# Kernel optimization log

Measured on AMD Instinct MI355X. Metric: run time of the kernel, lower is better.

Reference implementation:

```python
import jax, jax.numpy as jnp
import numpy as np

N_CUST = 500000
N_FUND = 50000
N_EDGE = 4000000
D_CUST = 101
D_FUND = 1
HID = 64


def setup_inputs() -> dict:
    key = jax.random.key(0)
    ks = jax.random.split(key, 16)
    s = lambda fan_in: 1.0 / np.sqrt(fan_in)
    return {
        "x_customer": jax.random.normal(ks[0], (N_CUST, D_CUST), jnp.float32),
        "x_fund": jax.random.normal(ks[1], (N_FUND, D_FUND), jnp.float32),
        "src_fund": jax.random.randint(ks[2], (N_EDGE,), 0, N_FUND, jnp.int64),
        "dst_customer": jax.random.randint(ks[3], (N_EDGE,), 0, N_CUST, jnp.int64),
        # per-node-type input projections
        "W_cust": jax.random.uniform(ks[4], (D_CUST, HID), jnp.float32, -s(D_CUST), s(D_CUST)),
        "b_cust": jax.random.uniform(ks[5], (HID,), jnp.float32, -s(D_CUST), s(D_CUST)),
        "W_fund": jax.random.uniform(ks[6], (D_FUND, HID), jnp.float32, -s(D_FUND), s(D_FUND)),
        "b_fund": jax.random.uniform(ks[7], (HID,), jnp.float32, -s(D_FUND), s(D_FUND)),
        # SAGEConv fund->customer: lin_l (neighbor aggr, bias) + lin_r (self, no bias)
        "W_l": jax.random.uniform(ks[8], (HID, HID), jnp.float32, -s(HID), s(HID)),
        "b_l": jax.random.uniform(ks[9], (HID,), jnp.float32, -s(HID), s(HID)),
        "W_r": jax.random.uniform(ks[10], (HID, HID), jnp.float32, -s(HID), s(HID)),
        # output head
        "W_out": jax.random.uniform(ks[11], (HID, 2), jnp.float32, -s(HID), s(HID)),
        "b_out": jax.random.uniform(ks[12], (2,), jnp.float32, -s(HID), s(HID)),
    }


def reference(x_customer, x_fund, src_fund, dst_customer,
              W_cust, b_cust, W_fund, b_fund, W_l, b_l, W_r, W_out, b_out):
    # per-node-type linear + relu
    h_c = jax.nn.relu(x_customer @ W_cust + b_cust)  # [N_CUST, HID]
    h_f = jax.nn.relu(x_fund @ W_fund + b_fund)      # [N_FUND, HID]

    # SAGEConv (fund -> customer): gather src fund features per edge,
    # mean-aggregate by destination customer (scatter-sum / count)
    msgs = h_f[src_fund]  # [N_EDGE, HID]
    summed = jax.ops.segment_sum(msgs, dst_customer, num_segments=N_CUST)
    cnt = jax.ops.segment_sum(jnp.ones((msgs.shape[0],), msgs.dtype),
                              dst_customer, num_segments=N_CUST)
    mean = summed / jnp.maximum(cnt, 1.0)[:, None]

    out_c = mean @ W_l + b_l + h_c @ W_r  # SAGE: lin_l(aggr) + lin_r(self)
    return out_c @ W_out + b_out          # [N_CUST, 2]
```

## Files before the change

kernel.cpp:

```cpp
#include <hip/hip_runtime.h>
#include <stdint.h>

#define N_CUST 500000
#define N_FUND 50000
#define N_EDGE 4000000
#define D_CUST 101
#define HID 64

#define NB   512
#define EPB  ((N_EDGE + NB - 1) / NB)
#define CB   1024
#define NBKT ((N_CUST + CB - 1) / CB)
#define TILES (N_CUST / 16)

typedef float  float4u __attribute__((ext_vector_type(4), aligned(4)));
using frag_ab = __attribute__((ext_vector_type(8))) short;
using frag_cd = __attribute__((ext_vector_type(4))) float;

struct __align__(16) Accum { float g0, g1, cnt, pad; };

__device__ __forceinline__ short f2bf(float f) {
    unsigned u = __float_as_uint(f);
    u += 0x7fffu + ((u >> 16) & 1u);
    return (short)(u >> 16);
}

__global__ __launch_bounds__(256) void k_prep(
    const float* __restrict__ W_r, const float* __restrict__ W_out,
    const float* __restrict__ b_l, const float* __restrict__ b_out,
    const float* __restrict__ W_l,
    float* __restrict__ Bt, float* __restrict__ Af, float* __restrict__ c2)
{
    int t = threadIdx.x;
    if (t < 128) {
        int h = t >> 1, j = t & 1;
        float s = 0.f, sa = 0.f;
        for (int k = 0; k < 64; ++k) {
            float wo = W_out[k * 2 + j];
            s  = fmaf(W_r[h * 64 + k], wo, s);
            sa = fmaf(W_l[h * 64 + k], wo, sa);
        }
        Bt[t] = s;
        Af[t] = sa;
    } else if (t < 130) {
        int j = t - 128;
        float s = b_out[j];
        for (int k = 0; k < 64; ++k)
            s = fmaf(b_l[k], W_out[k * 2 + j], s);
        c2[j] = s;
    }
}

__global__ __launch_bounds__(256) void k_gf(
    const float* __restrict__ x_fund,
    const float* __restrict__ W_fund,
    const float* __restrict__ b_fund,
    const float* __restrict__ Af,
    float2* __restrict__ gf)
{
    int f = blockIdx.x * 256 + threadIdx.x;
    if (f >= N_FUND) return;
    float xf = x_fund[f];
    float g0 = 0.f, g1 = 0.f;
    #pragma unroll
    for (int h = 0; h < 64; ++h) {
        float hf = fmaxf(fmaf(xf, W_fund[h], b_fund[h]), 0.f);
        g0 = fmaf(hf, Af[2 * h + 0], g0);
        g1 = fmaf(hf, Af[2 * h + 1], g1);
    }
    gf[f] = make_float2(g0, g1);
}

__global__ __launch_bounds__(256) void k_count(
    const int* __restrict__ dst, unsigned* __restrict__ cntTab)
{
    __shared__ unsigned hist[NBKT];
    int t = threadIdx.x, b = blockIdx.x;
    for (int k = t; k < NBKT; k += 256) hist[k] = 0;
    __syncthreads();
    int e0 = b * EPB, e1 = min(e0 + EPB, N_EDGE);
    for (int e = e0 + t; e < e1; e += 256)
        atomicAdd(&hist[((unsigned)dst[e]) >> 10], 1u);
    __syncthreads();
    for (int k = t; k < NBKT; k += 256) cntTab[(size_t)k * NB + b] = hist[k];
}

__global__ __launch_bounds__(256) void k_scan1(
    const unsigned* __restrict__ cntTab, unsigned* __restrict__ bktBase)
{
    __shared__ unsigned tot[NBKT];
    int t = threadIdx.x;
    for (int k = t; k < NBKT; k += 256) {
        unsigned s = 0;
        const unsigned* row = cntTab + (size_t)k * NB;
        for (int b = 0; b < NB; ++b) s += row[b];
        tot[k] = s;
    }
    __syncthreads();
    if (t < 64) {
        unsigned v[8], pre[8], run = 0;
        #pragma unroll
        for (int j = 0; j < 8; ++j) {
            int idx = t * 8 + j;
            v[j] = (idx < NBKT) ? tot[idx] : 0u;
            pre[j] = run; run += v[j];
        }
        unsigned sc = run;
        #pragma unroll
        for (int d = 1; d < 64; d <<= 1) {
            unsigned n = __shfl_up(sc, d, 64);
            if (t >= d) sc += n;
        }
        unsigned lane_excl = sc - run;
        #pragma unroll
        for (int j = 0; j < 8; ++j) {
            int idx = t * 8 + j;
            if (idx < NBKT) bktBase[idx] = lane_excl + pre[j];
        }
        if (t == 0) bktBase[NBKT] = N_EDGE;
    }
}

__global__ __launch_bounds__(64) void k_scan2(
    const unsigned* __restrict__ cntTab, const unsigned* __restrict__ bktBase,
    unsigned* __restrict__ offTab)
{
    int k = blockIdx.x, l = threadIdx.x;
    const unsigned* row = cntTab + (size_t)k * NB;
    unsigned v[8], pre[8], run = 0;
    #pragma unroll
    for (int j = 0; j < 8; ++j) { v[j] = row[l * 8 + j]; pre[j] = run; run += v[j]; }
    unsigned sc = run;
    #pragma unroll
    for (int d = 1; d < 64; d <<= 1) {
        unsigned n = __shfl_up(sc, d, 64);
        if (l >= d) sc += n;
    }
    unsigned base = bktBase[k] + (sc - run);
    unsigned* orow = offTab + (size_t)k * NB;
    #pragma unroll
    for (int j = 0; j < 8; ++j) orow[l * 8 + j] = base + pre[j];
}

__global__ __launch_bounds__(256) void k_reorder(
    const int* __restrict__ src, const int* __restrict__ dst,
    const unsigned* __restrict__ offTab, unsigned* __restrict__ recs)
{
    __shared__ unsigned cur[NBKT];
    int t = threadIdx.x, b = blockIdx.x;
    for (int k = t; k < NBKT; k += 256) cur[k] = offTab[(size_t)k * NB + b];
    __syncthreads();
    int e0 = b * EPB, e1 = min(e0 + EPB, N_EDGE);
    for (int e = e0 + t; e < e1; e += 256) {
        unsigned d = (unsigned)dst[e];
        unsigned s = (unsigned)src[e];
        unsigned pos = atomicAdd(&cur[d >> 10], 1u);
        recs[pos] = s | ((d & 1023u) << 16);
    }
}

__global__ __launch_bounds__(256) void k_aggregate(
    const unsigned* __restrict__ recs, const unsigned* __restrict__ bktBase,
    const float2* __restrict__ gf, float2* __restrict__ mean)
{
    __shared__ float s0[CB], s1[CB], scn[CB];
    int t = threadIdx.x, k = blockIdx.x;
    for (int c = t; c < CB; c += 256) { s0[c] = 0.f; s1[c] = 0.f; scn[c] = 0.f; }
    __syncthreads();
    unsigned r0 = bktBase[k], r1 = bktBase[k + 1];
    for (unsigned i = r0 + t; i < r1; i += 256) {
        unsigned r = recs[i];
        float2 g = gf[r & 0xFFFFu];
        unsigned dl = r >> 16;
        atomicAdd(&s0[dl], g.x);
        atomicAdd(&s1[dl], g.y);
        atomicAdd(&scn[dl], 1.f);
    }
    __syncthreads();
    int cust0 = k * CB;
    for (int c = t; c < CB; c += 256) {
        int cu = cust0 + c;
        if (cu < N_CUST) {
            float inv = 1.0f / fmaxf(scn[c], 1.0f);
            mean[cu] = make_float2(s0[c] * inv, s1[c] * inv);
        }
    }
}

__global__ __launch_bounds__(256) void k_scatter_direct(
    const int* __restrict__ src, const int* __restrict__ dst,
    const float2* __restrict__ gf, Accum* __restrict__ A)
{
    int stride = gridDim.x * 256;
    for (int e = blockIdx.x * 256 + threadIdx.x; e < N_EDGE; e += stride) {
        int s = src[e], d = dst[e];
        float2 g = gf[s];
        unsafeAtomicAdd(&A[d].g0, g.x);
        unsafeAtomicAdd(&A[d].g1, g.y);
        unsafeAtomicAdd(&A[d].cnt, 1.0f);
    }
}

template<bool USE_MEAN>
__global__ __launch_bounds__(256) void k_cust(
    const float* __restrict__ x, const float* __restrict__ Wc,
    const float* __restrict__ bc, const float* __restrict__ Bt,
    const float* __restrict__ c2,
    const float2* __restrict__ mean, const Accum* __restrict__ A,
    float2* __restrict__ out)
{
    __shared__ float zb[4][16 * 68];
    int tid = threadIdx.x;
    int w = tid >> 6, lane = tid & 63;
    int c = lane & 15, q = lane >> 4;
    float* z = zb[w];

    frag_ab bfrag[4][4];
    for (int nt = 0; nt < 4; ++nt)
        for (int kc = 0; kc < 4; ++kc) {
            frag_ab f;
            for (int j = 0; j < 8; ++j) {
                int k = kc * 32 + q * 8 + j;
                int h = nt * 16 + c;
                f[j] = (k < D_CUST) ? f2bf(Wc[k * HID + h]) : (short)0;
            }
            bfrag[nt][kc] = f;
        }
    float btv[32];
    #pragma unroll
    for (int j = 0; j < 8; ++j) {
        float4u v = *(const float4u*)(Bt + q * 32 + j * 4);
        btv[j*4+0] = v[0]; btv[j*4+1] = v[1]; btv[j*4+2] = v[2]; btv[j*4+3] = v[3];
    }
    float bcv[4];
    #pragma unroll
    for (int nt = 0; nt < 4; ++nt) bcv[nt] = bc[nt * 16 + c];
    float c20 = c2[0], c21 = c2[1];

    int wglob = blockIdx.x * 4 + w;
    int wstride = gridDim.x * 4;
    for (int t = wglob; t < TILES; t += wstride) {
        int row = t * 16 + c;
        const float* xr = x + (size_t)row * D_CUST;
        frag_ab af[4];
        #pragma unroll
        for (int kc = 0; kc < 3; ++kc) {
            float4u lo = *(const float4u*)(xr + kc * 32 + q * 8);
            float4u hi = *(const float4u*)(xr + kc * 32 + q * 8 + 4);
            frag_ab f;
            f[0]=f2bf(lo[0]); f[1]=f2bf(lo[1]); f[2]=f2bf(lo[2]); f[3]=f2bf(lo[3]);
            f[4]=f2bf(hi[0]); f[5]=f2bf(hi[1]); f[6]=f2bf(hi[2]); f[7]=f2bf(hi[3]);
            af[kc] = f;
        }
        {
            frag_ab f = {0,0,0,0,0,0,0,0};
            if (q == 0) {
                float4u lo = *(const float4u*)(xr + 96);
                f[0]=f2bf(lo[0]); f[1]=f2bf(lo[1]); f[2]=f2bf(lo[2]); f[3]=f2bf(lo[3]);
                f[4]=f2bf(xr[100]);
            }
            af[3] = f;
        }
        frag_cd acc[4];
        #pragma unroll
        for (int nt = 0; nt < 4; ++nt)
            acc[nt] = (frag_cd){bcv[nt], bcv[nt], bcv[nt], bcv[nt]};
        #pragma unroll
        for (int kc = 0; kc < 4; ++kc)
            #pragma unroll
            for (int nt = 0; nt < 4; ++nt)
                acc[nt] = __builtin_amdgcn_mfma_f32_16x16x32_bf16(
                    af[kc], bfrag[nt][kc], acc[nt], 0, 0, 0);

        #pragma unroll
        for (int nt = 0; nt < 4; ++nt)
            #pragma unroll
            for (int i = 0; i < 4; ++i)
                z[(q * 4 + i) * 68 + nt * 16 + c] = fmaxf(acc[nt][i], 0.f);

        float p0 = 0.f, p1 = 0.f;
        #pragma unroll
        for (int j4 = 0; j4 < 4; ++j4) {
            float4u zv = *(const float4u*)(z + c * 68 + q * 16 + j4 * 4);
            #pragma unroll
            for (int u = 0; u < 4; ++u) {
                int j = j4 * 4 + u;
                p0 = fmaf(zv[u], btv[2 * j + 0], p0);
                p1 = fmaf(zv[u], btv[2 * j + 1], p1);
            }
        }
        p0 += __shfl_xor(p0, 16, 64); p0 += __shfl_xor(p0, 32, 64);
        p1 += __shfl_xor(p1, 16, 64); p1 += __shfl_xor(p1, 32, 64);
        if (q == 0) {
            int orow = t * 16 + c;
            float m0, m1;
            if (USE_MEAN) {
                float2 m = mean[orow]; m0 = m.x; m1 = m.y;
            } else {
                Accum a = A[orow];
                float inv = 1.0f / fmaxf(a.cnt, 1.0f);
                m0 = a.g0 * inv; m1 = a.g1 * inv;
            }
            out[orow] = make_float2(p0 + m0 + c20, p1 + m1 + c21);
        }
    }
}

extern "C" void kernel_launch(void* const* d_in, const int* in_sizes, int n_in,
                              void* d_out, int out_size, void* d_ws, size_t ws_size,
                              hipStream_t stream) {
    const float* x_customer = (const float*)d_in[0];
    const float* x_fund     = (const float*)d_in[1];
    const int*   src_fund   = (const int*)d_in[2];
    const int*   dst_cust   = (const int*)d_in[3];
    const float* W_cust     = (const float*)d_in[4];
    const float* b_cust     = (const float*)d_in[5];
    const float* W_fund     = (const float*)d_in[6];
    const float* b_fund     = (const float*)d_in[7];
    const float* W_l        = (const float*)d_in[8];
    const float* b_l        = (const float*)d_in[9];
    const float* W_r        = (const float*)d_in[10];
    const float* W_out      = (const float*)d_in[11];
    const float* b_out      = (const float*)d_in[12];

    char* ws = (char*)d_ws;
    const size_t NEED = 22407424;

    if (ws_size >= NEED) {
        unsigned* cntTab  = (unsigned*)(ws);
        unsigned* offTab  = (unsigned*)(ws + 1001472);
        unsigned* bktBase = (unsigned*)(ws + 2002944);
        float2*   gf      = (float2*)  (ws + 2005248);
        float*    Bt      = (float*)   (ws + 2405248);
        float*    Af      = (float*)   (ws + 2405760);
        float*    c2      = (float*)   (ws + 2406272);
        float2*   mean    = (float2*)  (ws + 2406400);
        unsigned* recs    = (unsigned*)(ws + 6406400);

        k_prep<<<1, 256, 0, stream>>>(W_r, W_out, b_l, b_out, W_l, Bt, Af, c2);
        k_gf<<<(N_FUND + 255) / 256, 256, 0, stream>>>(x_fund, W_fund, b_fund, Af, gf);
        k_count<<<NB, 256, 0, stream>>>(dst_cust, cntTab);
        k_scan1<<<1, 256, 0, stream>>>(cntTab, bktBase);
        k_scan2<<<NBKT, 64, 0, stream>>>(cntTab, bktBase, offTab);
        k_reorder<<<NB, 256, 0, stream>>>(src_fund, dst_cust, offTab, recs);
        k_aggregate<<<NBKT, 256, 0, stream>>>(recs, bktBase, gf, mean);
        k_cust<true><<<768, 256, 0, stream>>>(
            x_customer, W_cust, b_cust, Bt, c2, mean, nullptr, (float2*)d_out);
    } else {
        Accum*  A  = (Accum*) (ws);
        float2* gf = (float2*)(ws + 8000000);
        float*  Bt = (float*) (ws + 8400000);
        float*  Af = (float*) (ws + 8400512);
        float*  c2 = (float*) (ws + 8401024);

        hipMemsetAsync(A, 0, sizeof(Accum) * (size_t)N_CUST, stream);
        k_prep<<<1, 256, 0, stream>>>(W_r, W_out, b_l, b_out, W_l, Bt, Af, c2);
        k_gf<<<(N_FUND + 255) / 256, 256, 0, stream>>>(x_fund, W_fund, b_fund, Af, gf);
        k_scatter_direct<<<2048, 256, 0, stream>>>(src_fund, dst_cust, gf, A);
        k_cust<false><<<768, 256, 0, stream>>>(
            x_customer, W_cust, b_cust, Bt, c2, nullptr, A, (float2*)d_out);
    }
}
```

Measured before the change: 516.1 us.

## Replace count/scan passes with fixed-capacity buckets and LDS-staged reorder

```diff
diff --git a/kernel.cpp b/kernel.cpp
--- a/kernel.cpp
+++ b/kernel.cpp
@@ -11,6 +11,7 @@
 #define EPB  ((N_EDGE + NB - 1) / NB)
 #define CB   1024
 #define NBKT ((N_CUST + CB - 1) / CB)
+#define CAP  16384
 #define TILES (N_CUST / 16)
 
 typedef float  float4u __attribute__((ext_vector_type(4), aligned(4)));
@@ -29,7 +30,8 @@
     const float* __restrict__ W_r, const float* __restrict__ W_out,
     const float* __restrict__ b_l, const float* __restrict__ b_out,
     const float* __restrict__ W_l,
-    float* __restrict__ Bt, float* __restrict__ Af, float* __restrict__ c2)
+    float* __restrict__ Bt, float* __restrict__ Af, float* __restrict__ c2,
+    unsigned* __restrict__ gcur)
 {
     int t = threadIdx.x;
     if (t < 128) {
@@ -49,6 +51,7 @@
             s = fmaf(b_l[k], W_out[k * 2 + j], s);
         c2[j] = s;
     }
+    for (int k = t; k < NBKT; k += 256) gcur[k] = (unsigned)k * CAP;
 }
 
 __global__ __launch_bounds__(256) void k_gf(
@@ -71,38 +74,33 @@
     gf[f] = make_float2(g0, g1);
 }
 
-__global__ __launch_bounds__(256) void k_count(
-    const int* __restrict__ dst, unsigned* __restrict__ cntTab)
+__global__ __launch_bounds__(256) void k_reorder(
+    const int* __restrict__ src, const int* __restrict__ dst,
+    unsigned* __restrict__ gcur, unsigned* __restrict__ recs)
 {
     __shared__ unsigned hist[NBKT];
+    __shared__ unsigned localOff[NBKT];
+    __shared__ unsigned cur[NBKT];
+    __shared__ unsigned baseG[NBKT];
+    __shared__ unsigned ldsRec[EPB];
+    __shared__ unsigned short ldsBkt[EPB];
+
     int t = threadIdx.x, b = blockIdx.x;
+    int e0 = b * EPB, e1 = min(e0 + EPB, N_EDGE);
+    int cntE = e1 - e0;
+
     for (int k = t; k < NBKT; k += 256) hist[k] = 0;
     __syncthreads();
-    int e0 = b * EPB, e1 = min(e0 + EPB, N_EDGE);
     for (int e = e0 + t; e < e1; e += 256)
         atomicAdd(&hist[((unsigned)dst[e]) >> 10], 1u);
     __syncthreads();
-    for (int k = t; k < NBKT; k += 256) cntTab[(size_t)k * NB + b] = hist[k];
-}
-
-__global__ __launch_bounds__(256) void k_scan1(
-    const unsigned* __restrict__ cntTab, unsigned* __restrict__ bktBase)
-{
-    __shared__ unsigned tot[NBKT];
-    int t = threadIdx.x;
-    for (int k = t; k < NBKT; k += 256) {
-        unsigned s = 0;
-        const unsigned* row = cntTab + (size_t)k * NB;
-        for (int b = 0; b < NB; ++b) s += row[b];
-        tot[k] = s;
-    }
-    __syncthreads();
+
     if (t < 64) {
         unsigned v[8], pre[8], run = 0;
         #pragma unroll
         for (int j = 0; j < 8; ++j) {
             int idx = t * 8 + j;
-            v[j] = (idx < NBKT) ? tot[idx] : 0u;
+            v[j] = (idx < NBKT) ? hist[idx] : 0u;
             pre[j] = run; run += v[j];
         }
         unsigned sc = run;
@@ -115,59 +113,45 @@
         #pragma unroll
         for (int j = 0; j < 8; ++j) {
             int idx = t * 8 + j;
-            if (idx < NBKT) bktBase[idx] = lane_excl + pre[j];
-        }
-        if (t == 0) bktBase[NBKT] = N_EDGE;
-    }
-}
-
-__global__ __launch_bounds__(64) void k_scan2(
-    const unsigned* __restrict__ cntTab, const unsigned* __restrict__ bktBase,
-    unsigned* __restrict__ offTab)
-{
-    int k = blockIdx.x, l = threadIdx.x;
-    const unsigned* row = cntTab + (size_t)k * NB;
-    unsigned v[8], pre[8], run = 0;
-    #pragma unroll
-    for (int j = 0; j < 8; ++j) { v[j] = row[l * 8 + j]; pre[j] = run; run += v[j]; }
-    unsigned sc = run;
-    #pragma unroll
-    for (int d = 1; d < 64; d <<= 1) {
-        unsigned n = __shfl_up(sc, d, 64);
-        if (l >= d) sc += n;
-    }
-    unsigned base = bktBase[k] + (sc - run);
-    unsigned* orow = offTab + (size_t)k * NB;
-    #pragma unroll
-    for (int j = 0; j < 8; ++j) orow[l * 8 + j] = base + pre[j];
-}
-
-__global__ __launch_bounds__(256) void k_reorder(
-    const int* __restrict__ src, const int* __restrict__ dst,
-    const unsigned* __restrict__ offTab, unsigned* __restrict__ recs)
-{
-    __shared__ unsigned cur[NBKT];
-    int t = threadIdx.x, b = blockIdx.x;
-    for (int k = t; k < NBKT; k += 256) cur[k] = offTab[(size_t)k * NB + b];
-    __syncthreads();
-    int e0 = b * EPB, e1 = min(e0 + EPB, N_EDGE);
+            if (idx < NBKT) {
+                localOff[idx] = lane_excl + pre[j];
+                cur[idx]      = lane_excl + pre[j];
+            }
+        }
+    }
+    __syncthreads();
+
+    for (int k = t; k < NBKT; k += 256) {
+        unsigned h = hist[k];
+        baseG[k] = h ? atomicAdd(&gcur[k], h) : 0u;
+    }
+
     for (int e = e0 + t; e < e1; e += 256) {
         unsigned d = (unsigned)dst[e];
         unsigned s = (unsigned)src[e];
-        unsigned pos = atomicAdd(&cur[d >> 10], 1u);
-        recs[pos] = s | ((d & 1023u) << 16);
+        unsigned k = d >> 10;
+        unsigned p = atomicAdd(&cur[k], 1u);
+        ldsRec[p] = s | ((d & 1023u) << 16);
+        ldsBkt[p] = (unsigned short)k;
+    }
+    __syncthreads();
+
+    for (int i = t; i < cntE; i += 256) {
+        unsigned k = ldsBkt[i];
+        unsigned g = baseG[k] + (i - localOff[k]);
+        recs[g] = ldsRec[i];
     }
 }
 
 __global__ __launch_bounds__(256) void k_aggregate(
-    const unsigned* __restrict__ recs, const unsigned* __restrict__ bktBase,
+    const unsigned* __restrict__ recs, const unsigned* __restrict__ gcur,
     const float2* __restrict__ gf, float2* __restrict__ mean)
 {
     __shared__ float s0[CB], s1[CB], scn[CB];
     int t = threadIdx.x, k = blockIdx.x;
     for (int c = t; c < CB; c += 256) { s0[c] = 0.f; s1[c] = 0.f; scn[c] = 0.f; }
     __syncthreads();
-    unsigned r0 = bktBase[k], r1 = bktBase[k + 1];
+    unsigned r0 = (unsigned)k * CAP, r1 = gcur[k];
     for (unsigned i = r0 + t; i < r1; i += 256) {
         unsigned r = recs[i];
         float2 g = gf[r & 0xFFFFu];
@@ -210,10 +194,13 @@
     float2* __restrict__ out)
 {
     __shared__ float zb[4][16 * 68];
+    __shared__ float sBt[128];
     int tid = threadIdx.x;
     int w = tid >> 6, lane = tid & 63;
     int c = lane & 15, q = lane >> 4;
     float* z = zb[w];
+
+    if (tid < 128) sBt[tid] = Bt[tid];
 
     frag_ab bfrag[4][4];
     for (int nt = 0; nt < 4; ++nt)
@@ -226,16 +213,11 @@
             }
             bfrag[nt][kc] = f;
         }
-    float btv[32];
-    #pragma unroll
-    for (int j = 0; j < 8; ++j) {
-        float4u v = *(const float4u*)(Bt + q * 32 + j * 4);
-        btv[j*4+0] = v[0]; btv[j*4+1] = v[1]; btv[j*4+2] = v[2]; btv[j*4+3] = v[3];
-    }
     float bcv[4];
     #pragma unroll
     for (int nt = 0; nt < 4; ++nt) bcv[nt] = bc[nt * 16 + c];
     float c20 = c2[0], c21 = c2[1];
+    __syncthreads();
 
     int wglob = blockIdx.x * 4 + w;
     int wstride = gridDim.x * 4;
@@ -282,12 +264,12 @@
         #pragma unroll
         for (int j4 = 0; j4 < 4; ++j4) {
             float4u zv = *(const float4u*)(z + c * 68 + q * 16 + j4 * 4);
-            #pragma unroll
-            for (int u = 0; u < 4; ++u) {
-                int j = j4 * 4 + u;
-                p0 = fmaf(zv[u], btv[2 * j + 0], p0);
-                p1 = fmaf(zv[u], btv[2 * j + 1], p1);
-            }
+            float4u b0 = *(const float4u*)(sBt + q * 32 + j4 * 8);
+            float4u b1 = *(const float4u*)(sBt + q * 32 + j4 * 8 + 4);
+            p0 = fmaf(zv[0], b0[0], p0); p1 = fmaf(zv[0], b0[1], p1);
+            p0 = fmaf(zv[1], b0[2], p0); p1 = fmaf(zv[1], b0[3], p1);
+            p0 = fmaf(zv[2], b1[0], p0); p1 = fmaf(zv[2], b1[1], p1);
+            p0 = fmaf(zv[3], b1[2], p0); p1 = fmaf(zv[3], b1[3], p1);
         }
         p0 += __shfl_xor(p0, 16, 64); p0 += __shfl_xor(p0, 32, 64);
         p1 += __shfl_xor(p1, 16, 64); p1 += __shfl_xor(p1, 32, 64);
@@ -324,40 +306,36 @@
     const float* b_out      = (const float*)d_in[12];
 
     char* ws = (char*)d_ws;
-    const size_t NEED = 22407424;
+    const size_t NEED = 4403456ull + (size_t)NBKT * CAP * 4ull + 64;
 
     if (ws_size >= NEED) {
-        unsigned* cntTab  = (unsigned*)(ws);
-        unsigned* offTab  = (unsigned*)(ws + 1001472);
-        unsigned* bktBase = (unsigned*)(ws + 2002944);
-        float2*   gf      = (float2*)  (ws + 2005248);
-        float*    Bt      = (float*)   (ws + 2405248);
-        float*    Af      = (float*)   (ws + 2405760);
-        float*    c2      = (float*)   (ws + 2406272);
-        float2*   mean    = (float2*)  (ws + 2406400);
-        unsigned* recs    = (unsigned*)(ws + 6406400);
-
-        k_prep<<<1, 256, 0, stream>>>(W_r, W_out, b_l, b_out, W_l, Bt, Af, c2);
+        float2*   gf   = (float2*)  (ws);
+        float*    Bt   = (float*)   (ws + 400000);
+        float*    Af   = (float*)   (ws + 400512);
+        float*    c2   = (float*)   (ws + 401024);
+        unsigned* gcur = (unsigned*)(ws + 401408);
+        float2*   mean = (float2*)  (ws + 403456);
+        unsigned* recs = (unsigned*)(ws + 4403456);
+
+        k_prep<<<1, 256, 0, stream>>>(W_r, W_out, b_l, b_out, W_l, Bt, Af, c2, gcur);
         k_gf<<<(N_FUND + 255) / 256, 256, 0, stream>>>(x_fund, W_fund, b_fund, Af, gf);
-        k_count<<<NB, 256, 0, stream>>>(dst_cust, cntTab);
-        k_scan1<<<1, 256, 0, stream>>>(cntTab, bktBase);
-        k_scan2<<<NBKT, 64, 0, stream>>>(cntTab, bktBase, offTab);
-        k_reorder<<<NB, 256, 0, stream>>>(src_fund, dst_cust, offTab, recs);
-        k_aggregate<<<NBKT, 256, 0, stream>>>(recs, bktBase, gf, mean);
-        k_cust<true><<<768, 256, 0, stream>>>(
+        k_reorder<<<NB, 256, 0, stream>>>(src_fund, dst_cust, gcur, recs);
+        k_aggregate<<<NBKT, 256, 0, stream>>>(recs, gcur, gf, mean);
+        k_cust<true><<<1024, 256, 0, stream>>>(
             x_customer, W_cust, b_cust, Bt, c2, mean, nullptr, (float2*)d_out);
     } else {
-        Accum*  A  = (Accum*) (ws);
-        float2* gf = (float2*)(ws + 8000000);
-        float*  Bt = (float*) (ws + 8400000);
-        float*  Af = (float*) (ws + 8400512);
-        float*  c2 = (float*) (ws + 8401024);
+        Accum*    A    = (Accum*) (ws);
+        float2*   gf   = (float2*)(ws + 8000000);
+        float*    Bt   = (float*) (ws + 8400000);
+        float*    Af   = (float*) (ws + 8400512);
+        float*    c2   = (float*) (ws + 8401024);
+        unsigned* gcur = (unsigned*)(ws + 8401408);
 
         hipMemsetAsync(A, 0, sizeof(Accum) * (size_t)N_CUST, stream);
-        k_prep<<<1, 256, 0, stream>>>(W_r, W_out, b_l, b_out, W_l, Bt, Af, c2);
+        k_prep<<<1, 256, 0, stream>>>(W_r, W_out, b_l, b_out, W_l, Bt, Af, c2, gcur);
         k_gf<<<(N_FUND + 255) / 256, 256, 0, stream>>>(x_fund, W_fund, b_fund, Af, gf);
         k_scatter_direct<<<2048, 256, 0, stream>>>(src_fund, dst_cust, gf, A);
-        k_cust<false><<<768, 256, 0, stream>>>(
+        k_cust<false><<<1024, 256, 0, stream>>>(
             x_customer, W_cust, b_cust, Bt, c2, nullptr, A, (float2*)d_out);
     }
 }
```

Measured after the change: 445.3 us. -13.7%, faster.
